# Kernel tuning notes

Hardware: AMD Instinct MI355X
Metric: run time of the kernel (lower is better)

The kernel has to match this reference:

```python
import jax, jax.numpy as jnp
import numpy as np
import math
from jax.scipy.special import logsumexp

B, S, D, H, L, FF, T, V = 32, 512, 512, 8, 2, 2048, 32, 32000
DH = D // H
LN_EPS = 1e-5
NEG = -1e9


def make_pe(seq_len, d_model):
    pos = np.arange(seq_len, dtype=np.float32)[:, None]
    div = np.exp(np.arange(0, d_model, 2, dtype=np.float32) * (-np.log(10000.0) / d_model))
    pe = np.zeros((seq_len, d_model), np.float32)
    pe[:, 0::2] = np.sin(pos * div)
    pe[:, 1::2] = np.cos(pos * div)
    return jnp.asarray(pe)


def layer_norm(x, scale, bias):
    mu = x.mean(-1, keepdims=True)
    var = ((x - mu) ** 2).mean(-1, keepdims=True)
    return (x - mu) / jnp.sqrt(var + LN_EPS) * scale + bias


def setup_inputs() -> dict:
    key = jax.random.key(0)
    ks = jax.random.split(key, 16)
    w = lambda k, shape, s=0.02: (jax.random.normal(k, shape, dtype=jnp.float32) * s)
    inp = {
        'tokens': jax.random.randint(ks[0], (B, S), 0, V),
        'tags': jax.random.randint(ks[1], (B, S), 0, T),
        'mask': jnp.ones((B, S), dtype=bool),
        'emb': w(ks[2], (V, D)),
        'Wqkv': w(ks[3], (L, 3 * D, D)),
        'bqkv': jnp.zeros((L, 3 * D), jnp.float32),
        'Wo': w(ks[4], (L, D, D)),
        'bo': jnp.zeros((L, D), jnp.float32),
        'ln1_s': jnp.ones((L, D), jnp.float32),
        'ln1_b': jnp.zeros((L, D), jnp.float32),
        'W1': w(ks[5], (L, FF, D)),
        'b1': jnp.zeros((L, FF), jnp.float32),
        'W2': w(ks[6], (L, D, FF)),
        'b2': jnp.zeros((L, D), jnp.float32),
        'ln2_s': jnp.ones((L, D), jnp.float32),
        'ln2_b': jnp.zeros((L, D), jnp.float32),
        'Wtag': w(ks[7], (T, D)),
        'btag': jnp.zeros((T,), jnp.float32),
        'trans': w(ks[8], (T, T), 0.1),
        'start_t': w(ks[9], (T,), 0.1),
        'end_t': w(ks[10], (T,), 0.1),
    }
    return inp


def _forward(tokens, tags, mask, emb, Wqkv, bqkv, Wo, bo, ln1_s, ln1_b, W1, b1, W2, b2,
             ln2_s, ln2_b, Wtag, btag, trans, start_t, end_t):
    # --- embedding + positional encoding ---
    x = emb[tokens] + make_pe(S, D)[None]  # [B,S,D]
    # --- transformer encoder (post-norm, relu, batch_first) ---
    for l in range(L):
        qkv = x @ Wqkv[l].T + bqkv[l]
        q, k, v = jnp.split(qkv, 3, axis=-1)
        q = q.reshape(B, S, H, DH).transpose(0, 2, 1, 3)
        k = k.reshape(B, S, H, DH).transpose(0, 2, 1, 3)
        v = v.reshape(B, S, H, DH).transpose(0, 2, 1, 3)
        scores = jnp.einsum('bhqd,bhkd->bhqk', q, k) / math.sqrt(DH)
        scores = jnp.where(mask[:, None, None, :], scores, NEG)  # key padding mask
        attn = jax.nn.softmax(scores, axis=-1)
        o = jnp.einsum('bhqk,bhkd->bhqd', attn, v).transpose(0, 2, 1, 3).reshape(B, S, D)
        x = layer_norm(x + o @ Wo[l].T + bo[l], ln1_s[l], ln1_b[l])
        h = jax.nn.relu(x @ W1[l].T + b1[l])
        x = layer_norm(x + h @ W2[l].T + b2[l], ln2_s[l], ln2_b[l])
    emissions = x @ Wtag.T + btag  # [B,S,T]

    maskf = mask.astype(emissions.dtype)
    # --- gold path score ---
    emit_sel = jnp.take_along_axis(emissions, tags[..., None], axis=2)[..., 0]  # [B,S]
    trans_sel = trans[tags[:, :-1], tags[:, 1:]]  # [B,S-1]
    score = start_t[tags[:, 0]] + emit_sel[:, 0]
    score = score + jnp.sum((trans_sel + emit_sel[:, 1:]) * maskf[:, 1:], axis=1)
    last_pos = mask.astype(jnp.int32).sum(axis=1) - 1
    last_tags = jnp.take_along_axis(tags, last_pos[:, None], axis=1)[:, 0]
    score = score + end_t[last_tags]

    # --- log partition: forward algorithm as a scan over time ---
    alpha0 = start_t[None] + emissions[:, 0]  # [B,T]

    def step(alpha, inp):
        emit_t, m_t = inp  # [B,T], [B]
        new = logsumexp(alpha[:, :, None] + trans[None] + emit_t[:, None, :], axis=1)
        alpha = jnp.where(m_t[:, None], new, alpha)
        return alpha, None

    alpha, _ = jax.lax.scan(step, alpha0,
                            (emissions[:, 1:].transpose(1, 0, 2), mask[:, 1:].T))
    log_z = logsumexp(alpha + end_t[None], axis=1)
    return (log_z - score).mean()


def reference(tokens, tags, mask, emb, Wqkv, bqkv, Wo, bo, ln1_s, ln1_b, W1, b1, W2, b2,
              ln2_s, ln2_b, Wtag, btag, trans, start_t, end_t):
    return _forward(tokens, tags, mask, emb, Wqkv, bqkv, Wo, bo, ln1_s, ln1_b, W1, b1,
                    W2, b2, ln2_s, ln2_b, Wtag, btag, trans, start_t, end_t)
```

## Files before the change

### kernel.cpp

```cpp
#include <hip/hip_runtime.h>

#define Bz 32
#define Sz 512
#define Dz 512
#define Hz 8
#define Lz 2
#define FFz 2048
#define Tz 32
#define DHz 64

typedef unsigned short u16;
typedef __attribute__((ext_vector_type(8))) short short8;
typedef __attribute__((ext_vector_type(4))) short short4v;
typedef __attribute__((ext_vector_type(4))) float f32x4;

__device__ __forceinline__ float b2f(u16 s) {
    union { unsigned u; float f; } x; x.u = ((unsigned)s) << 16; return x.f;
}
__device__ __forceinline__ u16 f2b(float f) {
    union { float f; unsigned u; } x; x.f = f;
    unsigned r = x.u + 0x7FFFu + ((x.u >> 16) & 1u);
    return (u16)(r >> 16);
}

__device__ __forceinline__ void gload_lds16(const void* g, void* l) {
    __builtin_amdgcn_global_load_lds((const __attribute__((address_space(1))) void*)g,
                                     (__attribute__((address_space(3))) void*)l, 16, 0, 0);
}

template<int BM, int BN, bool OUT_BF16, bool RELU>
__global__ __launch_bounds__(256) void gemm_k(
    const u16* __restrict__ A, int lda, long sAb, long sAh,
    const u16* __restrict__ Bm, int ldb, long sBb, long sBh,
    void* __restrict__ Cm, int ldc, long sCb, long sCh,
    const float* __restrict__ bias,
    const u16* __restrict__ res, int ldres,
    float scale, int K, int nh)
{
    constexpr int WM = BM / 2, WN = BN / 2;
    constexpr int TM = WM / 16, TN = WN / 16;
    __shared__ __align__(16) u16 ldsA[BM * 64];
    __shared__ __align__(16) u16 ldsB[BN * 64];

    const int tid = threadIdx.x, lane = tid & 63, w = tid >> 6;
    const int wm = w >> 1, wn = w & 1;
    const int z = blockIdx.z, zb = z / nh, zh = z % nh;
    A  += (size_t)zb * sAb + (size_t)zh * sAh;
    Bm += (size_t)zb * sBb + (size_t)zh * sBh;
    char* Cc = (char*)Cm + ((size_t)zb * sCb + (size_t)zh * sCh) * (OUT_BF16 ? 2 : 4);

    const int m0 = blockIdx.y * BM, n0 = blockIdx.x * BN;
    f32x4 acc[TM][TN];
#pragma unroll
    for (int mi = 0; mi < TM; ++mi)
#pragma unroll
        for (int ni = 0; ni < TN; ++ni) acc[mi][ni] = (f32x4){0.f, 0.f, 0.f, 0.f};

    const int sr = lane >> 3;
    const int scsw = (((lane & 7) ^ sr) << 3);

    for (int k0 = 0; k0 < K; k0 += 64) {
        const int ra = w * (BM / 4);
#pragma unroll
        for (int t = 0; t < BM / 32; ++t) {
            const u16* g = A + (size_t)(m0 + ra + t * 8 + sr) * lda + k0 + scsw;
            gload_lds16(g, &ldsA[(ra + t * 8) * 64]);
        }
        const int rb = w * (BN / 4);
#pragma unroll
        for (int t = 0; t < BN / 32; ++t) {
            const u16* g = Bm + (size_t)(n0 + rb + t * 8 + sr) * ldb + k0 + scsw;
            gload_lds16(g, &ldsB[(rb + t * 8) * 64]);
        }
        asm volatile("s_waitcnt vmcnt(0)" ::: "memory");
        __syncthreads();
#pragma unroll
        for (int kk = 0; kk < 64; kk += 32) {
            const int kc = (kk >> 3) + (lane >> 4);
            const int sw = ((kc ^ (lane & 7)) << 3);
            short8 af[TM], bf[TN];
#pragma unroll
            for (int mi = 0; mi < TM; ++mi)
                af[mi] = *(const short8*)&ldsA[(wm * WM + mi * 16 + (lane & 15)) * 64 + sw];
#pragma unroll
            for (int ni = 0; ni < TN; ++ni)
                bf[ni] = *(const short8*)&ldsB[(wn * WN + ni * 16 + (lane & 15)) * 64 + sw];
#pragma unroll
            for (int mi = 0; mi < TM; ++mi)
#pragma unroll
                for (int ni = 0; ni < TN; ++ni)
                    acc[mi][ni] = __builtin_amdgcn_mfma_f32_16x16x32_bf16(bf[ni], af[mi], acc[mi][ni], 0, 0, 0);
        }
        __syncthreads();
    }
#pragma unroll
    for (int mi = 0; mi < TM; ++mi) {
        const int m = m0 + wm * WM + mi * 16 + (lane & 15);
#pragma unroll
        for (int ni = 0; ni < TN; ++ni) {
            const int n = n0 + wn * WN + ni * 16 + ((lane >> 4) << 2);
            float v0 = acc[mi][ni][0] * scale, v1 = acc[mi][ni][1] * scale;
            float v2 = acc[mi][ni][2] * scale, v3 = acc[mi][ni][3] * scale;
            if (bias) {
                const float4 b4 = *(const float4*)&bias[n];
                v0 += b4.x; v1 += b4.y; v2 += b4.z; v3 += b4.w;
            }
            if (res) {
                const short4v r4 = *(const short4v*)&res[(size_t)m * ldres + n];
                v0 += b2f((u16)r4[0]); v1 += b2f((u16)r4[1]);
                v2 += b2f((u16)r4[2]); v3 += b2f((u16)r4[3]);
            }
            if (RELU) {
                v0 = fmaxf(v0, 0.f); v1 = fmaxf(v1, 0.f);
                v2 = fmaxf(v2, 0.f); v3 = fmaxf(v3, 0.f);
            }
            if (OUT_BF16) {
                short4v pk;
                pk[0] = (short)f2b(v0); pk[1] = (short)f2b(v1);
                pk[2] = (short)f2b(v2); pk[3] = (short)f2b(v3);
                *(short4v*)&((u16*)Cc)[(size_t)m * ldc + n] = pk;
            } else {
                f32x4 o = (f32x4){v0, v1, v2, v3};
                *(f32x4*)&((float*)Cc)[(size_t)m * ldc + n] = o;
            }
        }
    }
}

__global__ __launch_bounds__(256) void attn_k(const u16* __restrict__ qkv,
                                              const u16* __restrict__ vt,
                                              u16* __restrict__ ao)
{
    __shared__ __align__(16) u16 ldsP[4][32 * 40];
    const int tid = threadIdx.x, lane = tid & 63, w = tid >> 6;
    const int z = blockIdx.x, qt = blockIdx.y;
    const int bb = z >> 3, hh = z & 7;
    const int quad = lane >> 4, c = lane & 15;
    u16* myP = ldsP[w];
    const int q0 = qt * 128 + w * 32;

    const u16* qbase = qkv + (size_t)(bb * Sz + q0) * 1536 + hh * 64;
    short8 qf[2][2];
#pragma unroll
    for (int ni = 0; ni < 2; ++ni)
#pragma unroll
        for (int kk = 0; kk < 2; ++kk)
            qf[ni][kk] = *(const short8*)(qbase + (size_t)(ni * 16 + c) * 1536 + kk * 32 + quad * 8);

    f32x4 oacc[4][2];
    float mst[2] = {-1e30f, -1e30f}, lst[2] = {0.f, 0.f};
#pragma unroll
    for (int i = 0; i < 4; ++i)
#pragma unroll
        for (int j2 = 0; j2 < 2; ++j2) oacc[i][j2] = (f32x4){0.f, 0.f, 0.f, 0.f};

    const u16* kbase = qkv + (size_t)(bb * Sz) * 1536 + 512 + hh * 64;
    const u16* vbase = vt + (size_t)z * (64 * 512);

#pragma unroll 2
    for (int jt = 0; jt < 16; ++jt) {
        const int kv0 = jt * 32;
        short8 kf[2][2];
#pragma unroll
        for (int mi = 0; mi < 2; ++mi)
#pragma unroll
            for (int kk = 0; kk < 2; ++kk)
                kf[mi][kk] = *(const short8*)(kbase + (size_t)(kv0 + mi * 16 + c) * 1536 + kk * 32 + quad * 8);
        f32x4 sacc[2][2];
#pragma unroll
        for (int mi = 0; mi < 2; ++mi)
#pragma unroll
            for (int ni = 0; ni < 2; ++ni) sacc[mi][ni] = (f32x4){0.f, 0.f, 0.f, 0.f};
#pragma unroll
        for (int kk = 0; kk < 2; ++kk)
#pragma unroll
            for (int mi = 0; mi < 2; ++mi)
#pragma unroll
                for (int ni = 0; ni < 2; ++ni)
                    sacc[mi][ni] = __builtin_amdgcn_mfma_f32_16x16x32_bf16(kf[mi][kk], qf[ni][kk], sacc[mi][ni], 0, 0, 0);
        float mnew[2], alpha[2], lad[2];
#pragma unroll
        for (int ni = 0; ni < 2; ++ni) {
            float v = -1e30f;
#pragma unroll
            for (int mi = 0; mi < 2; ++mi)
#pragma unroll
                for (int r = 0; r < 4; ++r) v = fmaxf(v, sacc[mi][ni][r]);
            v *= 0.125f;
            v = fmaxf(v, __shfl_xor(v, 16));
            v = fmaxf(v, __shfl_xor(v, 32));
            mnew[ni] = fmaxf(mst[ni], v);
            alpha[ni] = __expf(mst[ni] - mnew[ni]);
            mst[ni] = mnew[ni];
            lad[ni] = 0.f;
        }
#pragma unroll
        for (int mi = 0; mi < 2; ++mi)
#pragma unroll
            for (int ni = 0; ni < 2; ++ni) {
                float p0 = __expf(sacc[mi][ni][0] * 0.125f - mnew[ni]);
                float p1 = __expf(sacc[mi][ni][1] * 0.125f - mnew[ni]);
                float p2 = __expf(sacc[mi][ni][2] * 0.125f - mnew[ni]);
                float p3 = __expf(sacc[mi][ni][3] * 0.125f - mnew[ni]);
                lad[ni] += (p0 + p1) + (p2 + p3);
                short4v pk;
                pk[0] = (short)f2b(p0); pk[1] = (short)f2b(p1);
                pk[2] = (short)f2b(p2); pk[3] = (short)f2b(p3);
                *(short4v*)&myP[(ni * 16 + c) * 40 + mi * 16 + quad * 4] = pk;
            }
#pragma unroll
        for (int ni = 0; ni < 2; ++ni) {
            float v = lad[ni];
            v += __shfl_xor(v, 16);
            v += __shfl_xor(v, 32);
            lst[ni] = lst[ni] * alpha[ni] + v;
        }
#pragma unroll
        for (int mi2 = 0; mi2 < 4; ++mi2)
#pragma unroll
            for (int ni = 0; ni < 2; ++ni) {
                oacc[mi2][ni][0] *= alpha[ni]; oacc[mi2][ni][1] *= alpha[ni];
                oacc[mi2][ni][2] *= alpha[ni]; oacc[mi2][ni][3] *= alpha[ni];
            }
        short8 vf[4], pf[2];
#pragma unroll
        for (int mi2 = 0; mi2 < 4; ++mi2)
            vf[mi2] = *(const short8*)(vbase + (size_t)(mi2 * 16 + c) * 512 + kv0 + quad * 8);
#pragma unroll
        for (int ni = 0; ni < 2; ++ni)
            pf[ni] = *(const short8*)&myP[(ni * 16 + c) * 40 + quad * 8];
#pragma unroll
        for (int mi2 = 0; mi2 < 4; ++mi2)
#pragma unroll
            for (int ni = 0; ni < 2; ++ni)
                oacc[mi2][ni] = __builtin_amdgcn_mfma_f32_16x16x32_bf16(vf[mi2], pf[ni], oacc[mi2][ni], 0, 0, 0);
    }
    float Linv[2] = {1.f / lst[0], 1.f / lst[1]};
#pragma unroll
    for (int mi2 = 0; mi2 < 4; ++mi2)
#pragma unroll
        for (int ni = 0; ni < 2; ++ni) {
            int q = q0 + ni * 16 + c;
            short4v pk;
#pragma unroll
            for (int r = 0; r < 4; ++r)
                pk[r] = (short)f2b(oacc[mi2][ni][r] * Linv[ni]);
            *(short4v*)&ao[(size_t)(bb * Sz + q) * 512 + hh * 64 + mi2 * 16 + quad * 4] = pk;
        }
}

__global__ __launch_bounds__(256) void prep_k(
    const float* __restrict__ Wqkv, const float* __restrict__ Wo,
    const float* __restrict__ W1, const float* __restrict__ W2,
    const float* __restrict__ wt, const float* __restrict__ bt,
    u16* __restrict__ wqkvb, u16* __restrict__ wob, u16* __restrict__ w1b,
    u16* __restrict__ w2b, u16* __restrict__ wtp, float* __restrict__ btp)
{
    const long n1 = (long)2 * 1536 * 512;
    const long n2 = n1 + (long)2 * 512 * 512;
    const long n3 = n2 + (long)2 * 2048 * 512;
    const long n4 = n3 + (long)2 * 512 * 2048;
    const long n5 = n4 + (long)64 * 512;
    long i = (long)blockIdx.x * 256 + threadIdx.x;
    if (i < n1) wqkvb[i] = f2b(Wqkv[i]);
    else if (i < n2) { long j = i - n1; wob[j] = f2b(Wo[j]); }
    else if (i < n3) { long j = i - n2; w1b[j] = f2b(W1[j]); }
    else if (i < n4) { long j = i - n3; w2b[j] = f2b(W2[j]); }
    else if (i < n5) { long j = i - n4; wtp[j] = ((j >> 9) < Tz) ? f2b(wt[j]) : (u16)0; }
    else if (i < n5 + 64) { long j = i - n5; btp[j] = (j < Tz) ? bt[j] : 0.f; }
}

__global__ __launch_bounds__(256) void embed_k(const int* __restrict__ tokens, const float* __restrict__ emb,
                                               u16* __restrict__ xb) {
    int bs = blockIdx.x * 4 + (threadIdx.x >> 6);
    int lane = threadIdx.x & 63;
    int s = bs & (Sz - 1);
    int tok = tokens[bs];
    const float* er = emb + (size_t)tok * Dz + lane * 8;
    float4 e0 = *(const float4*)er, e1 = *(const float4*)(er + 4);
    float e[8] = {e0.x, e0.y, e0.z, e0.w, e1.x, e1.y, e1.z, e1.w};
    short8 ov;
#pragma unroll
    for (int q = 0; q < 8; ++q) {
        int d = lane * 8 + q;
        int i2 = d & ~1;
        float div = expf(-(float)i2 * (9.210340371976184f / (float)Dz));
        float arg = (float)s * div;
        float pe = (d & 1) ? cosf(arg) : sinf(arg);
        ov[q] = (short)f2b(e[q] + pe);
    }
    *(short8*)&xb[(size_t)bs * Dz + lane * 8] = ov;
}

__global__ __launch_bounds__(256) void ln_k(const float* __restrict__ y, const float* __restrict__ sc,
                                            const float* __restrict__ bi, u16* __restrict__ xb) {
    int row = blockIdx.x * 4 + (threadIdx.x >> 6);
    int lane = threadIdx.x & 63;
    const float* yr = y + (size_t)row * Dz + lane * 8;
    float4 a = *(const float4*)yr, b = *(const float4*)(yr + 4);
    float v[8] = {a.x, a.y, a.z, a.w, b.x, b.y, b.z, b.w};
    float sum = 0.f, sq = 0.f;
#pragma unroll
    for (int q = 0; q < 8; ++q) { sum += v[q]; sq += v[q] * v[q]; }
    for (int o = 32; o; o >>= 1) { sum += __shfl_xor(sum, o); sq += __shfl_xor(sq, o); }
    float mu = sum * (1.f / Dz);
    float var = sq * (1.f / Dz) - mu * mu;
    float rstd = rsqrtf(var + 1e-5f);
    float4 s0 = *(const float4*)&sc[lane * 8], s1 = *(const float4*)&sc[lane * 8 + 4];
    float4 b0 = *(const float4*)&bi[lane * 8], b1 = *(const float4*)&bi[lane * 8 + 4];
    float scv[8] = {s0.x, s0.y, s0.z, s0.w, s1.x, s1.y, s1.z, s1.w};
    float biv[8] = {b0.x, b0.y, b0.z, b0.w, b1.x, b1.y, b1.z, b1.w};
    short8 ov;
#pragma unroll
    for (int q = 0; q < 8; ++q)
        ov[q] = (short)f2b((v[q] - mu) * rstd * scv[q] + biv[q]);
    *(short8*)&xb[(size_t)row * Dz + lane * 8] = ov;
}

__global__ __launch_bounds__(256) void transpose_v_k(const u16* __restrict__ qkv, u16* __restrict__ vt) {
    __shared__ u16 tile[64][72];
    int z = blockIdx.y; int bb = z >> 3, hh = z & 7;
    int s0 = blockIdx.x * 64;
    int t = threadIdx.x;
#pragma unroll
    for (int it = 0; it < 2; ++it) {
        int idx = it * 256 + t;
        int sl = idx >> 3, dv = idx & 7;
        const u16* g = qkv + (size_t)(bb * Sz + s0 + sl) * (3 * Dz) + 2 * Dz + hh * 64 + dv * 8;
        short8 vv = *(const short8*)g;
#pragma unroll
        for (int j = 0; j < 8; ++j) tile[sl][dv * 8 + j] = (u16)vv[j];
    }
    __syncthreads();
#pragma unroll
    for (int it = 0; it < 2; ++it) {
        int idx = it * 256 + t;
        int dh = idx >> 3, sv = idx & 7;
        short8 ov;
#pragma unroll
        for (int j = 0; j < 8; ++j) ov[j] = (short)tile[sv * 8 + j][dh];
        *(short8*)&vt[(size_t)z * DHz * Sz + (size_t)dh * Sz + s0 + sv * 8] = ov;
    }
}

__global__ __launch_bounds__(64) void crf_span_k(
    const float* __restrict__ emis, const float* __restrict__ trans,
    float* __restrict__ Pout, float* __restrict__ lsout)
{
    __shared__ __align__(16) u16 Pm[32 * 40];
    const int lane = threadIdx.x;
    const int b = blockIdx.y, s = blockIdx.x;
    const int t0 = 1 + 32 * s;
    const int tend = min(Sz - 1, t0 + 31);
    const int quad = lane >> 4, c = lane & 15;
    const float* em = emis + (size_t)b * Sz * 128;

    float ebf[2][8];
#pragma unroll
    for (int cj = 0; cj < 2; ++cj)
#pragma unroll
        for (int jj = 0; jj < 8; ++jj)
            ebf[cj][jj] = __expf(trans[(quad * 8 + jj) * 32 + cj * 16 + c]);

    {
        int i = lane >> 1;
        int jb = (lane & 1) * 16;
#pragma unroll
        for (int q = 0; q < 16; ++q) {
            int j = jb + q;
            float v = __expf(trans[i * 32 + j]) * __expf(em[(size_t)t0 * 128 + j]);
            Pm[i * 40 + j] = f2b(v);
        }
    }
    __syncthreads();

    float smax = 1.f, lsum = 0.f;
    float e0 = em[(size_t)(t0 + 1) * 128 + c];
    float e1 = em[(size_t)(t0 + 1) * 128 + 16 + c];
    for (int t = t0 + 1; t <= tend; ++t) {
        float rinv = 1.f / smax;
        float s0 = __expf(e0) * rinv, s1 = __expf(e1) * rinv;
        if (t < tend) {
            e0 = em[(size_t)(t + 1) * 128 + c];
            e1 = em[(size_t)(t + 1) * 128 + 16 + c];
        }
        short8 mb[2];
#pragma unroll
        for (int jj = 0; jj < 8; ++jj) {
            mb[0][jj] = (short)f2b(ebf[0][jj] * s0);
            mb[1][jj] = (short)f2b(ebf[1][jj] * s1);
        }
        short8 pa[2];
        pa[0] = *(const short8*)&Pm[c * 40 + quad * 8];
        pa[1] = *(const short8*)&Pm[(16 + c) * 40 + quad * 8];
        f32x4 C[2][2];
#pragma unroll
        for (int ri = 0; ri < 2; ++ri)
#pragma unroll
            for (int cj = 0; cj < 2; ++cj)
                C[ri][cj] = __builtin_amdgcn_mfma_f32_16x16x32_bf16(
                    pa[ri], mb[cj], (f32x4){0.f, 0.f, 0.f, 0.f}, 0, 0, 0);
        float bm = -1e30f;
#pragma unroll
        for (int ri = 0; ri < 2; ++ri)
#pragma unroll
            for (int cj = 0; cj < 2; ++cj)
#pragma unroll
                for (int r = 0; r < 4; ++r) bm = fmaxf(bm, C[ri][cj][r]);
        for (int o = 32; o; o >>= 1) bm = fmaxf(bm, __shfl_xor(bm, o));
        lsum += __logf(smax);
        smax = bm;
        __syncthreads();
        if (t < tend) {
#pragma unroll
            for (int ri = 0; ri < 2; ++ri)
#pragma unroll
                for (int cj = 0; cj < 2; ++cj)
#pragma unroll
                    for (int r = 0; r < 4; ++r) {
                        int i = ri * 16 + quad * 4 + r;
                        int j = cj * 16 + c;
                        Pm[i * 40 + j] = f2b(C[ri][cj][r]);
                    }
            __syncthreads();
        } else {
            float* Po = Pout + (((size_t)b * 16 + s) * 1024);
#pragma unroll
            for (int ri = 0; ri < 2; ++ri)
#pragma unroll
                for (int cj = 0; cj < 2; ++cj)
#pragma unroll
                    for (int r = 0; r < 4; ++r) {
                        int i = ri * 16 + quad * 4 + r;
                        int j = cj * 16 + c;
                        Po[i * 32 + j] = C[ri][cj][r];
                    }
        }
    }
    if (lane == 0) lsout[b * 16 + s] = lsum;
}

__global__ __launch_bounds__(64) void crf2_k(
    const float* __restrict__ emis, const int* __restrict__ tags,
    const float* __restrict__ trans, const float* __restrict__ start_t,
    const float* __restrict__ end_t, const float* __restrict__ Pspan,
    const float* __restrict__ lsspan, float* __restrict__ diff)
{
    const int b = blockIdx.x, lane = threadIdx.x;
    const int* tg = tags + b * Sz;
    const float* em = emis + (size_t)b * Sz * 128;
    float partial = 0.f;
    for (int t = 1 + lane; t < Sz; t += 64) {
        int tp = tg[t - 1], tc = tg[t];
        partial += trans[tp * Tz + tc] + em[(size_t)t * 128 + tc];
    }
    for (int o = 32; o; o >>= 1) partial += __shfl_xor(partial, o);
    float score = partial + start_t[tg[0]] + em[tg[0]] + end_t[tg[Sz - 1]];

    const int j = lane & 31, hb = lane & 32;
    float a0 = start_t[j] + em[j];
    float m0 = a0;
    for (int o = 16; o; o >>= 1) m0 = fmaxf(m0, __shfl_xor(m0, o));
    float a = __expf(a0 - m0);
    float ls = m0;

    const float* Pb_ = Pspan + (size_t)b * 16 * 1024;
    float Pc[32];
#pragma unroll
    for (int k = 0; k < 32; ++k) Pc[k] = Pb_[k * 32 + j];
    for (int s = 0; s < 16; ++s) {
        float Pn[32];
        if (s < 15) {
#pragma unroll
            for (int k = 0; k < 32; ++k) Pn[k] = Pb_[(s + 1) * 1024 + k * 32 + j];
        }
        float an = 0.f;
#pragma unroll
        for (int k = 0; k < 32; ++k) an += __shfl(a, hb + k) * Pc[k];
        float am = an;
        for (int o = 16; o; o >>= 1) am = fmaxf(am, __shfl_xor(am, o));
        a = an / am;
        ls += __logf(am) + lsspan[b * 16 + s];
#pragma unroll
        for (int k = 0; k < 32; ++k) Pc[k] = Pn[k];
    }
    float wv = a * __expf(end_t[j]);
    for (int o = 16; o; o >>= 1) wv += __shfl_xor(wv, o);
    float logz = ls + __logf(wv);
    if (lane == 0) diff[b] = logz - score;
}

__global__ __launch_bounds__(64) void reduce_k(const float* __restrict__ diff, float* __restrict__ out) {
    int lane = threadIdx.x;
    float v = (lane < Bz) ? diff[lane] : 0.f;
    for (int o = 32; o; o >>= 1) v += __shfl_xor(v, o);
    if (lane == 0) out[0] = v / (float)Bz;
}

__global__ void sentinel_k(float* out, float v) {
    if (threadIdx.x == 0) out[0] = v;
}

extern "C" void kernel_launch(void* const* d_in, const int* in_sizes, int n_in,
                              void* d_out, int out_size, void* d_ws, size_t ws_size,
                              hipStream_t stream) {
    const int*   tokens = (const int*)d_in[0];
    const int*   tags   = (const int*)d_in[1];
    const float* emb    = (const float*)d_in[3];
    const float* Wqkv   = (const float*)d_in[4];
    const float* bqkv   = (const float*)d_in[5];
    const float* Wo     = (const float*)d_in[6];
    const float* bo     = (const float*)d_in[7];
    const float* ln1s   = (const float*)d_in[8];
    const float* ln1b   = (const float*)d_in[9];
    const float* W1     = (const float*)d_in[10];
    const float* b1     = (const float*)d_in[11];
    const float* W2     = (const float*)d_in[12];
    const float* b2     = (const float*)d_in[13];
    const float* ln2s   = (const float*)d_in[14];
    const float* ln2b   = (const float*)d_in[15];
    const float* Wtag   = (const float*)d_in[16];
    const float* btag   = (const float*)d_in[17];
    const float* trans  = (const float*)d_in[18];
    const float* start_t= (const float*)d_in[19];
    const float* end_t  = (const float*)d_in[20];

    char* base = (char*)d_ws;
    size_t off = 0;
    auto alloc = [&](size_t bytes) -> void* {
        void* p = base + off;
        off += (bytes + 255) & ~(size_t)255;
        return p;
    };
    u16*   xb    = (u16*)  alloc((size_t)16384 * 512 * 2);
    u16*   qkv   = (u16*)  alloc((size_t)16384 * 1536 * 2);
    u16*   vt    = (u16*)  alloc((size_t)256 * 64 * 512 * 2);
    u16*   ao    = (u16*)  alloc((size_t)16384 * 512 * 2);
    u16*   wqkvb = (u16*)  alloc((size_t)2 * 1536 * 512 * 2);
    u16*   wob   = (u16*)  alloc((size_t)2 * 512 * 512 * 2);
    u16*   w1b   = (u16*)  alloc((size_t)2 * 2048 * 512 * 2);
    u16*   w2b   = (u16*)  alloc((size_t)2 * 512 * 2048 * 2);
    u16*   wtagb = (u16*)  alloc((size_t)64 * 512 * 2);
    float* btagp = (float*)alloc(256);
    float* diff  = (float*)alloc(256);
    u16*   scratch=(u16*)  alloc((size_t)16384 * 2048 * 2);
    float* y     = (float*)qkv;
    float* emis  = (float*)ao;
    float* Pspan = (float*)scratch;
    float* lsspan= (float*)(scratch + 1048576);

    if (off > ws_size) {
        sentinel_k<<<1, 64, 0, stream>>>((float*)d_out, (float)ws_size);
        return;
    }

    {
        long total = (long)2 * 1536 * 512 + (long)2 * 512 * 512 + (long)2 * 2048 * 512
                   + (long)2 * 512 * 2048 + (long)64 * 512 + 64;
        prep_k<<<(int)((total + 255) / 256), 256, 0, stream>>>(
            Wqkv, Wo, W1, W2, Wtag, btag, wqkvb, wob, w1b, w2b, wtagb, btagp);
    }
    embed_k<<<4096, 256, 0, stream>>>(tokens, emb, xb);

    for (int l = 0; l < Lz; ++l) {
        gemm_k<128, 128, true, false><<<dim3(12, 128, 1), 256, 0, stream>>>(
            xb, 512, 0, 0, wqkvb + (size_t)l * 1536 * 512, 512, 0, 0,
            qkv, 1536, 0, 0, bqkv + l * 1536, nullptr, 0, 1.f, 512, 1);
        transpose_v_k<<<dim3(8, 256), 256, 0, stream>>>(qkv, vt);
        attn_k<<<dim3(256, 4), 256, 0, stream>>>(qkv, vt, ao);
        gemm_k<128, 128, false, false><<<dim3(4, 128, 1), 256, 0, stream>>>(
            ao, 512, 0, 0, wob + (size_t)l * 512 * 512, 512, 0, 0,
            y, 512, 0, 0, bo + l * 512, xb, 512, 1.f, 512, 1);
        ln_k<<<4096, 256, 0, stream>>>(y, ln1s + l * 512, ln1b + l * 512, xb);
        gemm_k<128, 128, true, true><<<dim3(16, 128, 1), 256, 0, stream>>>(
            xb, 512, 0, 0, w1b + (size_t)l * 2048 * 512, 512, 0, 0,
            scratch, 2048, 0, 0, b1 + l * 2048, nullptr, 0, 1.f, 512, 1);
        gemm_k<128, 128, false, false><<<dim3(4, 128, 1), 256, 0, stream>>>(
            scratch, 2048, 0, 0, w2b + (size_t)l * 512 * 2048, 2048, 0, 0,
            y, 512, 0, 0, b2 + l * 512, xb, 512, 1.f, 2048, 1);
        ln_k<<<4096, 256, 0, stream>>>(y, ln2s + l * 512, ln2b + l * 512, xb);
    }
    gemm_k<128, 64, false, false><<<dim3(1, 128, 1), 256, 0, stream>>>(
        xb, 512, 0, 0, wtagb, 512, 0, 0,
        emis, 128, 0, 0, btagp, nullptr, 0, 1.f, 512, 1);
    crf_span_k<<<dim3(16, Bz), 64, 0, stream>>>(emis, trans, Pspan, lsspan);
    crf2_k<<<Bz, 64, 0, stream>>>(emis, tags, trans, start_t, end_t, Pspan, lsspan, diff);
    reduce_k<<<1, 64, 0, stream>>>(diff, (float*)d_out);
}
```

Baseline: 745.7 us.

## Fuse V transpose into QKV GEMM epilogue and streamline attention softmax

The QKV GEMM epilogue now writes the V columns straight into the transposed per-head layout, so the separate transpose kernel and its launch go away. The attention kernel also changes in several ways. It prefetches the next K tile during the current step and uses exp2 with a pre-scaled log2e/sqrt(d) constant and an fma. It rescales the accumulator and running sum only when a row max actually increases, and it truncates P to bf16 instead of rounding. The V stores in the epilogue are now scattered 2-byte writes with stride 512, and truncation adds a small rounding bias.

```diff
diff --git a/kernel.cpp b/kernel.cpp
--- a/kernel.cpp
+++ b/kernel.cpp
@@ -22,20 +22,24 @@
     unsigned r = x.u + 0x7FFFu + ((x.u >> 16) & 1u);
     return (u16)(r >> 16);
 }
+__device__ __forceinline__ u16 f2bt(float f) {
+    union { float f; unsigned u; } x; x.f = f;
+    return (u16)(x.u >> 16);
+}
 
 __device__ __forceinline__ void gload_lds16(const void* g, void* l) {
     __builtin_amdgcn_global_load_lds((const __attribute__((address_space(1))) void*)g,
                                      (__attribute__((address_space(3))) void*)l, 16, 0, 0);
 }
 
-template<int BM, int BN, bool OUT_BF16, bool RELU>
+template<int BM, int BN, bool OUT_BF16, bool RELU, bool VT>
 __global__ __launch_bounds__(256) void gemm_k(
     const u16* __restrict__ A, int lda, long sAb, long sAh,
     const u16* __restrict__ Bm, int ldb, long sBb, long sBh,
     void* __restrict__ Cm, int ldc, long sCb, long sCh,
     const float* __restrict__ bias,
     const u16* __restrict__ res, int ldres,
-    float scale, int K, int nh)
+    float scale, int K, int nh, u16* __restrict__ vtp)
 {
     constexpr int WM = BM / 2, WN = BN / 2;
     constexpr int TM = WM / 16, TN = WN / 16;
@@ -114,7 +118,13 @@
                 v0 = fmaxf(v0, 0.f); v1 = fmaxf(v1, 0.f);
                 v2 = fmaxf(v2, 0.f); v3 = fmaxf(v3, 0.f);
             }
-            if (OUT_BF16) {
+            if (VT && n >= 1024) {
+                const int hh = (n - 1024) >> 6, dh0 = (n - 1024) & 63;
+                const int bb = m >> 9, s = m & 511;
+                u16* vp = vtp + (((size_t)(bb * 8 + hh) * 64 + dh0) * 512 + s);
+                vp[0]    = f2b(v0); vp[512]  = f2b(v1);
+                vp[1024] = f2b(v2); vp[1536] = f2b(v3);
+            } else if (OUT_BF16) {
                 short4v pk;
                 pk[0] = (short)f2b(v0); pk[1] = (short)f2b(v1);
                 pk[2] = (short)f2b(v2); pk[3] = (short)f2b(v3);
@@ -132,6 +142,7 @@
                                               u16* __restrict__ ao)
 {
     __shared__ __align__(16) u16 ldsP[4][32 * 40];
+    const float SC = 0.18033688011f;
     const int tid = threadIdx.x, lane = tid & 63, w = tid >> 6;
     const int z = blockIdx.x, qt = blockIdx.y;
     const int bb = z >> 3, hh = z & 7;
@@ -148,7 +159,7 @@
             qf[ni][kk] = *(const short8*)(qbase + (size_t)(ni * 16 + c) * 1536 + kk * 32 + quad * 8);
 
     f32x4 oacc[4][2];
-    float mst[2] = {-1e30f, -1e30f}, lst[2] = {0.f, 0.f};
+    float m2[2] = {-1e30f, -1e30f}, lst[2] = {0.f, 0.f};
 #pragma unroll
     for (int i = 0; i < 4; ++i)
 #pragma unroll
@@ -156,16 +167,17 @@
 
     const u16* kbase = qkv + (size_t)(bb * Sz) * 1536 + 512 + hh * 64;
     const u16* vbase = vt + (size_t)z * (64 * 512);
+
+    short8 kf[2][2];
+#pragma unroll
+    for (int mi = 0; mi < 2; ++mi)
+#pragma unroll
+        for (int kk = 0; kk < 2; ++kk)
+            kf[mi][kk] = *(const short8*)(kbase + (size_t)(mi * 16 + c) * 1536 + kk * 32 + quad * 8);
 
 #pragma unroll 2
     for (int jt = 0; jt < 16; ++jt) {
         const int kv0 = jt * 32;
-        short8 kf[2][2];
-#pragma unroll
-        for (int mi = 0; mi < 2; ++mi)
-#pragma unroll
-            for (int kk = 0; kk < 2; ++kk)
-                kf[mi][kk] = *(const short8*)(kbase + (size_t)(kv0 + mi * 16 + c) * 1536 + kk * 32 + quad * 8);
         f32x4 sacc[2][2];
 #pragma unroll
         for (int mi = 0; mi < 2; ++mi)
@@ -178,7 +190,14 @@
 #pragma unroll
                 for (int ni = 0; ni < 2; ++ni)
                     sacc[mi][ni] = __builtin_amdgcn_mfma_f32_16x16x32_bf16(kf[mi][kk], qf[ni][kk], sacc[mi][ni], 0, 0, 0);
-        float mnew[2], alpha[2], lad[2];
+        if (jt < 15) {
+#pragma unroll
+            for (int mi = 0; mi < 2; ++mi)
+#pragma unroll
+                for (int kk = 0; kk < 2; ++kk)
+                    kf[mi][kk] = *(const short8*)(kbase + (size_t)(kv0 + 32 + mi * 16 + c) * 1536 + kk * 32 + quad * 8);
+        }
+        float mn[2], al[2];
 #pragma unroll
         for (int ni = 0; ni < 2; ++ni) {
             float v = -1e30f;
@@ -186,42 +205,45 @@
             for (int mi = 0; mi < 2; ++mi)
 #pragma unroll
                 for (int r = 0; r < 4; ++r) v = fmaxf(v, sacc[mi][ni][r]);
-            v *= 0.125f;
             v = fmaxf(v, __shfl_xor(v, 16));
             v = fmaxf(v, __shfl_xor(v, 32));
-            mnew[ni] = fmaxf(mst[ni], v);
-            alpha[ni] = __expf(mst[ni] - mnew[ni]);
-            mst[ni] = mnew[ni];
-            lad[ni] = 0.f;
-        }
+            mn[ni] = fmaxf(m2[ni], v * SC);
+            al[ni] = exp2f(m2[ni] - mn[ni]);
+        }
+        const bool need = (mn[0] > m2[0]) | (mn[1] > m2[1]);
+        m2[0] = mn[0]; m2[1] = mn[1];
+        float lad[2] = {0.f, 0.f};
 #pragma unroll
         for (int mi = 0; mi < 2; ++mi)
 #pragma unroll
             for (int ni = 0; ni < 2; ++ni) {
-                float p0 = __expf(sacc[mi][ni][0] * 0.125f - mnew[ni]);
-                float p1 = __expf(sacc[mi][ni][1] * 0.125f - mnew[ni]);
-                float p2 = __expf(sacc[mi][ni][2] * 0.125f - mnew[ni]);
-                float p3 = __expf(sacc[mi][ni][3] * 0.125f - mnew[ni]);
+                float p0 = exp2f(fmaf(sacc[mi][ni][0], SC, -mn[ni]));
+                float p1 = exp2f(fmaf(sacc[mi][ni][1], SC, -mn[ni]));
+                float p2 = exp2f(fmaf(sacc[mi][ni][2], SC, -mn[ni]));
+                float p3 = exp2f(fmaf(sacc[mi][ni][3], SC, -mn[ni]));
                 lad[ni] += (p0 + p1) + (p2 + p3);
                 short4v pk;
-                pk[0] = (short)f2b(p0); pk[1] = (short)f2b(p1);
-                pk[2] = (short)f2b(p2); pk[3] = (short)f2b(p3);
+                pk[0] = (short)f2bt(p0); pk[1] = (short)f2bt(p1);
+                pk[2] = (short)f2bt(p2); pk[3] = (short)f2bt(p3);
                 *(short4v*)&myP[(ni * 16 + c) * 40 + mi * 16 + quad * 4] = pk;
             }
+        if (__any(need)) {
+#pragma unroll
+            for (int mi2 = 0; mi2 < 4; ++mi2)
+#pragma unroll
+                for (int ni = 0; ni < 2; ++ni) {
+                    oacc[mi2][ni][0] *= al[ni]; oacc[mi2][ni][1] *= al[ni];
+                    oacc[mi2][ni][2] *= al[ni]; oacc[mi2][ni][3] *= al[ni];
+                }
+            lst[0] *= al[0]; lst[1] *= al[1];
+        }
 #pragma unroll
         for (int ni = 0; ni < 2; ++ni) {
             float v = lad[ni];
             v += __shfl_xor(v, 16);
             v += __shfl_xor(v, 32);
-            lst[ni] = lst[ni] * alpha[ni] + v;
-        }
-#pragma unroll
-        for (int mi2 = 0; mi2 < 4; ++mi2)
-#pragma unroll
-            for (int ni = 0; ni < 2; ++ni) {
-                oacc[mi2][ni][0] *= alpha[ni]; oacc[mi2][ni][1] *= alpha[ni];
-                oacc[mi2][ni][2] *= alpha[ni]; oacc[mi2][ni][3] *= alpha[ni];
-            }
+            lst[ni] += v;
+        }
         short8 vf[4], pf[2];
 #pragma unroll
         for (int mi2 = 0; mi2 < 4; ++mi2)
@@ -315,32 +337,6 @@
     for (int q = 0; q < 8; ++q)
         ov[q] = (short)f2b((v[q] - mu) * rstd * scv[q] + biv[q]);
     *(short8*)&xb[(size_t)row * Dz + lane * 8] = ov;
-}
-
-__global__ __launch_bounds__(256) void transpose_v_k(const u16* __restrict__ qkv, u16* __restrict__ vt) {
-    __shared__ u16 tile[64][72];
-    int z = blockIdx.y; int bb = z >> 3, hh = z & 7;
-    int s0 = blockIdx.x * 64;
-    int t = threadIdx.x;
-#pragma unroll
-    for (int it = 0; it < 2; ++it) {
-        int idx = it * 256 + t;
-        int sl = idx >> 3, dv = idx & 7;
-        const u16* g = qkv + (size_t)(bb * Sz + s0 + sl) * (3 * Dz) + 2 * Dz + hh * 64 + dv * 8;
-        short8 vv = *(const short8*)g;
-#pragma unroll
-        for (int j = 0; j < 8; ++j) tile[sl][dv * 8 + j] = (u16)vv[j];
-    }
-    __syncthreads();
-#pragma unroll
-    for (int it = 0; it < 2; ++it) {
-        int idx = it * 256 + t;
-        int dh = idx >> 3, sv = idx & 7;
-        short8 ov;
-#pragma unroll
-        for (int j = 0; j < 8; ++j) ov[j] = (short)tile[sv * 8 + j][dh];
-        *(short8*)&vt[(size_t)z * DHz * Sz + (size_t)dh * Sz + s0 + sv * 8] = ov;
-    }
 }
 
 __global__ __launch_bounds__(64) void crf_span_k(
@@ -563,26 +559,25 @@
     embed_k<<<4096, 256, 0, stream>>>(tokens, emb, xb);
 
     for (int l = 0; l < Lz; ++l) {
-        gemm_k<128, 128, true, false><<<dim3(12, 128, 1), 256, 0, stream>>>(
+        gemm_k<128, 128, true, false, true><<<dim3(12, 128, 1), 256, 0, stream>>>(
             xb, 512, 0, 0, wqkvb + (size_t)l * 1536 * 512, 512, 0, 0,
-            qkv, 1536, 0, 0, bqkv + l * 1536, nullptr, 0, 1.f, 512, 1);
-        transpose_v_k<<<dim3(8, 256), 256, 0, stream>>>(qkv, vt);
+            qkv, 1536, 0, 0, bqkv + l * 1536, nullptr, 0, 1.f, 512, 1, vt);
         attn_k<<<dim3(256, 4), 256, 0, stream>>>(qkv, vt, ao);
-        gemm_k<128, 128, false, false><<<dim3(4, 128, 1), 256, 0, stream>>>(
+        gemm_k<128, 128, false, false, false><<<dim3(4, 128, 1), 256, 0, stream>>>(
             ao, 512, 0, 0, wob + (size_t)l * 512 * 512, 512, 0, 0,
-            y, 512, 0, 0, bo + l * 512, xb, 512, 1.f, 512, 1);
+            y, 512, 0, 0, bo + l * 512, xb, 512, 1.f, 512, 1, nullptr);
         ln_k<<<4096, 256, 0, stream>>>(y, ln1s + l * 512, ln1b + l * 512, xb);
-        gemm_k<128, 128, true, true><<<dim3(16, 128, 1), 256, 0, stream>>>(
+        gemm_k<128, 128, true, true, false><<<dim3(16, 128, 1), 256, 0, stream>>>(
             xb, 512, 0, 0, w1b + (size_t)l * 2048 * 512, 512, 0, 0,
-            scratch, 2048, 0, 0, b1 + l * 2048, nullptr, 0, 1.f, 512, 1);
-        gemm_k<128, 128, false, false><<<dim3(4, 128, 1), 256, 0, stream>>>(
+            scratch, 2048, 0, 0, b1 + l * 2048, nullptr, 0, 1.f, 512, 1, nullptr);
+        gemm_k<128, 128, false, false, false><<<dim3(4, 128, 1), 256, 0, stream>>>(
             scratch, 2048, 0, 0, w2b + (size_t)l * 512 * 2048, 2048, 0, 0,
-            y, 512, 0, 0, b2 + l * 512, xb, 512, 1.f, 2048, 1);
+            y, 512, 0, 0, b2 + l * 512, xb, 512, 1.f, 2048, 1, nullptr);
         ln_k<<<4096, 256, 0, stream>>>(y, ln2s + l * 512, ln2b + l * 512, xb);
     }
-    gemm_k<128, 64, false, false><<<dim3(1, 128, 1), 256, 0, stream>>>(
+    gemm_k<128, 64, false, false, false><<<dim3(1, 128, 1), 256, 0, stream>>>(
         xb, 512, 0, 0, wtagb, 512, 0, 0,
-        emis, 128, 0, 0, btagp, nullptr, 0, 1.f, 512, 1);
+        emis, 128, 0, 0, btagp, nullptr, 0, 1.f, 512, 1, nullptr);
     crf_span_k<<<dim3(16, Bz), 64, 0, stream>>>(emis, trans, Pspan, lsspan);
     crf2_k<<<Bz, 64, 0, stream>>>(emis, tags, trans, start_t, end_t, Pspan, lsspan, diff);
     reduce_k<<<1, 64, 0, stream>>>(diff, (float*)d_out);
```

After: 762.7 us. 1.02x slower.
